# Kernel optimization log

Hardware: AMD Instinct MI355X
Metric: run time of the kernel (lower is better)

## Reference

```python
import jax, jax.numpy as jnp
import numpy as np

B, H, W, C, NC = 4, 64, 64, 64, 19


def setup_inputs() -> dict:
    key = jax.random.key(0)
    ks = jax.random.split(key, 12)
    s = 0.05  # small init so sigmoid scores are not saturated
    return {
        "feature": jax.random.normal(ks[0], (B, H, W, C), dtype=jnp.float32),
        "predict": jax.random.normal(ks[1], (B, H, W, NC), dtype=jnp.float32),
        # height attention params (dim = H); k_linear in source is unused (q reused as k)
        "hq_w": jax.random.normal(ks[2], (H, H), dtype=jnp.float32) * s,
        "hq_b": jnp.zeros((H,), dtype=jnp.float32),
        "hv_w": jax.random.normal(ks[3], (H, H), dtype=jnp.float32) * s,
        "hv_b": jnp.zeros((H,), dtype=jnp.float32),
        # width attention params (dim = W)
        "wq_w": jax.random.normal(ks[4], (W, W), dtype=jnp.float32) * s,
        "wq_b": jnp.zeros((W,), dtype=jnp.float32),
        "wv_w": jax.random.normal(ks[5], (W, W), dtype=jnp.float32) * s,
        "wv_b": jnp.zeros((W,), dtype=jnp.float32),
        # gating scalars (nn.Parameter(torch.zeros(1)) in source; random here to exercise path)
        "h_gate": jax.random.normal(ks[6], (1,), dtype=jnp.float32) * 0.5,
        "w_gate": jax.random.normal(ks[7], (1,), dtype=jnp.float32) * 0.5,
        # 1x1 conv num_classes -> 1 (stored as [NC, 1] matrix; 1x1 conv == per-pixel linear)
        "conv_w": jax.random.normal(ks[8], (NC, 1), dtype=jnp.float32) * s,
        "conv_b": jnp.zeros((1,), dtype=jnp.float32),
    }


def _self_atten(x, wq, bq, wv, bv, dim):
    # Source uses q_linear for BOTH q and k (k_linear dead), softmax replaced by sigmoid.
    q = x @ wq + bq                                   # [B, N, dim]
    v = x @ wv + bv                                   # [B, N, dim]
    scores = jax.nn.sigmoid(jnp.einsum('bnd,bmd->bnm', q, q) / jnp.sqrt(jnp.float32(dim)))
    return jnp.einsum('bnm,bmd->bnd', scores, v)      # [B, N, dim]


def _axial(x, hq_w, hq_b, hv_w, hv_b, wq_w, wq_b, wv_w, wv_b, h_gate, w_gate):
    b, h, w, c = x.shape
    # height attention: seq = W*C, feature dim = H
    xh = x.transpose(0, 2, 3, 1).reshape(b, w * c, h)
    xh = _self_atten(xh, hq_w, hq_b, hv_w, hv_b, h)
    xh = xh.reshape(b, w, c, h).transpose(0, 3, 1, 2)  # back to [B,H,W,C]
    x = xh * h_gate + x
    # width attention: seq = H*C, feature dim = W
    xw = x.transpose(0, 1, 3, 2).reshape(b, h * c, w)
    xw = _self_atten(xw, wq_w, wq_b, wv_w, wv_b, w)
    xw = xw.reshape(b, h, c, w).transpose(0, 1, 3, 2)  # back to [B,H,W,C]
    x = xw * w_gate + x
    return x


def reference(feature, predict, hq_w, hq_b, hv_w, hv_b, wq_w, wq_b, wv_w, wv_b,
              h_gate, w_gate, conv_w, conv_b):
    feat = feature + _axial(feature, hq_w, hq_b, hv_w, hv_b,
                            wq_w, wq_b, wv_w, wv_b, h_gate, w_gate)
    p = 1.0 - jax.nn.sigmoid(predict)                 # [B,H,W,NC]
    p = p @ conv_w + conv_b                           # 1x1 conv -> [B,H,W,1]
    return p * feat                                   # broadcast gate -> [B,H,W,C]
```

## Files before the change

kernel.cpp:

```cpp
#include <hip/hip_runtime.h>

typedef _Float16 f16x8 __attribute__((ext_vector_type(8)));
typedef __fp16   fp16x2 __attribute__((ext_vector_type(2)));
typedef float f32x16 __attribute__((ext_vector_type(16)));

__device__ __forceinline__ unsigned pkrtz(float a, float b) {
    fp16x2 h = __builtin_amdgcn_cvt_pkrtz(a, b);
    union { fp16x2 h; unsigned u; } c; c.h = h; return c.u;
}

__device__ __forceinline__ unsigned short f2h(float f) {
    _Float16 h = (_Float16)f;
    union { _Float16 h; unsigned short s; } c; c.h = h; return c.s;
}

__device__ __forceinline__ f16x8 pack8(const float* v) {
    union { unsigned u[4]; f16x8 h; } c;
    c.u[0] = pkrtz(v[0], v[1]);
    c.u[1] = pkrtz(v[2], v[3]);
    c.u[2] = pkrtz(v[4], v[5]);
    c.u[3] = pkrtz(v[6], v[7]);
    return c.h;
}

__global__ __launch_bounds__(256) void prep_kernel(
    const float* __restrict__ src,
    const float* __restrict__ wq, const float* __restrict__ bq,
    const float* __restrict__ wv, const float* __restrict__ bv,
    unsigned short* __restrict__ Qg, unsigned short* __restrict__ Vtg)
{
    __shared__ float slab[64][65];
    __shared__ float wqs[4160];
    __shared__ float wvs[4160];

    const int t  = threadIdx.x;
    const int bx = blockIdx.x, b = blockIdx.y;
    const int lane = t & 63, w = t >> 6;
    const int l32 = lane & 31, hi = lane >> 5;

    {
        const float4* wq4 = (const float4*)wq;
        const float4* wv4 = (const float4*)wv;
        float4* q4 = (float4*)wqs; float4* v4 = (float4*)wvs;
        #pragma unroll
        for (int i = 0; i < 4; ++i) {
            q4[i*256 + t] = wq4[i*256 + t];
            v4[i*256 + t] = wv4[i*256 + t];
        }
    }
    {
        const int k = t >> 2, c0 = (t & 3) << 4;
        const size_t sb = (size_t)b*262144 + (size_t)k*4096 + (size_t)bx*64 + c0;
        #pragma unroll
        for (int i = 0; i < 4; ++i)
            *(float4*)&slab[k][c0 + i*4] = *(const float4*)&src[sb + i*4];
    }
    __syncthreads();

    const int mt = w >> 1, nt = w & 1;
    f16x8 xa[4], wqb[4], wvb[4];
    #pragma unroll
    for (int s = 0; s < 4; ++s) {
        const int k0 = s*16 + hi*8;
        float av[8], qv[8], vv[8];
        #pragma unroll
        for (int jj = 0; jj < 8; ++jj) {
            av[jj] = slab[k0 + jj][mt*32 + l32];
            qv[jj] = wqs[(k0 + jj)*64 + nt*32 + l32];
            vv[jj] = wvs[(k0 + jj)*64 + nt*32 + l32];
        }
        xa[s]  = pack8(av);
        wqb[s] = pack8(qv);
        wvb[s] = pack8(vv);
    }

    f32x16 fz;
    #pragma unroll
    for (int i = 0; i < 16; ++i) fz[i] = 0.f;
    f32x16 accQ = __builtin_amdgcn_mfma_f32_32x32x16_f16(xa[0], wqb[0], fz, 0,0,0);
    f32x16 accV = __builtin_amdgcn_mfma_f32_32x32x16_f16(xa[0], wvb[0], fz, 0,0,0);
    #pragma unroll
    for (int s = 1; s < 4; ++s) {
        accQ = __builtin_amdgcn_mfma_f32_32x32x16_f16(xa[s], wqb[s], accQ, 0,0,0);
        accV = __builtin_amdgcn_mfma_f32_32x32x16_f16(xa[s], wvb[s], accV, 0,0,0);
    }

    __syncthreads();

    {
        #pragma unroll
        for (int r = 0; r < 16; ++r) {
            const int crow = mt*32 + (r&3) + 8*(r>>2) + 4*hi;
            wqs[crow*65 + nt*32 + l32] = accQ[r];
            wvs[crow*65 + nt*32 + l32] = accV[r];
        }
    }
    __syncthreads();

    const int c = t & 63, jg = t >> 6;
    float qa[16], va[16];
    #pragma unroll
    for (int jj = 0; jj < 16; ++jj) {
        qa[jj] = bq[jg*16+jj] + wqs[c*65 + jg*16 + jj];
        va[jj] = bv[jg*16+jj] + wvs[c*65 + jg*16 + jj];
    }
    const int token = bx*64 + c;
    union { unsigned u[8]; uint4 v[2]; } qp;
    #pragma unroll
    for (int jj = 0; jj < 8; ++jj) qp.u[jj] = pkrtz(qa[2*jj], qa[2*jj+1]);
    const size_t qoff = ((size_t)b*4096 + token)*64 + jg*16;
    *(uint4*)&Qg[qoff]     = qp.v[0];
    *(uint4*)&Qg[qoff + 8] = qp.v[1];
    #pragma unroll
    for (int jj = 0; jj < 16; ++jj)
        Vtg[((size_t)b*64 + jg*16 + jj)*4096 + token] = f2h(va[jj]);
}

__global__ __launch_bounds__(256) void prep_w_kernel(
    const float* __restrict__ feature, const float* __restrict__ Pin,
    const float* __restrict__ gate,
    const float* __restrict__ wq, const float* __restrict__ bq,
    const float* __restrict__ wv, const float* __restrict__ bv,
    unsigned short* __restrict__ Qg, unsigned short* __restrict__ Vtg,
    float* __restrict__ x1out, int nsplit)
{
    __shared__ float slab[64][65];
    __shared__ float wqs[4160];
    __shared__ float wvs[4160];

    const int t  = threadIdx.x;
    const int bx = blockIdx.x, b = blockIdx.y;
    const int lane = t & 63, w = t >> 6;
    const int l32 = lane & 31, hi = lane >> 5;

    {
        const float4* wq4 = (const float4*)wq;
        const float4* wv4 = (const float4*)wv;
        float4* q4 = (float4*)wqs; float4* v4 = (float4*)wvs;
        #pragma unroll
        for (int i = 0; i < 4; ++i) {
            q4[i*256 + t] = wq4[i*256 + t];
            v4[i*256 + t] = wv4[i*256 + t];
        }
    }
    {
        const int k = t >> 2, c0 = (t & 3) << 4;
        const size_t off = (size_t)bx*4096 + (size_t)k*64 + c0;
        const size_t fb  = (size_t)b*262144 + off;
        const float g = gate[0];
        #pragma unroll
        for (int i = 0; i < 4; ++i) {
            float4 v  = *(const float4*)&feature[fb + i*4];
            float sx = 0.f, sy = 0.f, sz = 0.f, sw = 0.f;
            for (int ks = 0; ks < nsplit; ++ks) {
                float4 pk = *(const float4*)&Pin[((size_t)(ks*4 + b) << 18) + off + i*4];
                sx += pk.x; sy += pk.y; sz += pk.z; sw += pk.w;
            }
            v.x += g * sx; v.y += g * sy; v.z += g * sz; v.w += g * sw;
            *(float4*)&slab[k][c0 + i*4] = v;
            *(float4*)&x1out[fb + i*4] = v;
        }
    }
    __syncthreads();

    const int mt = w >> 1, nt = w & 1;
    f16x8 xa[4], wqb[4], wvb[4];
    #pragma unroll
    for (int s = 0; s < 4; ++s) {
        const int k0 = s*16 + hi*8;
        float av[8], qv[8], vv[8];
        #pragma unroll
        for (int jj = 0; jj < 8; ++jj) {
            av[jj] = slab[k0 + jj][mt*32 + l32];
            qv[jj] = wqs[(k0 + jj)*64 + nt*32 + l32];
            vv[jj] = wvs[(k0 + jj)*64 + nt*32 + l32];
        }
        xa[s]  = pack8(av);
        wqb[s] = pack8(qv);
        wvb[s] = pack8(vv);
    }

    f32x16 fz;
    #pragma unroll
    for (int i = 0; i < 16; ++i) fz[i] = 0.f;
    f32x16 accQ = __builtin_amdgcn_mfma_f32_32x32x16_f16(xa[0], wqb[0], fz, 0,0,0);
    f32x16 accV = __builtin_amdgcn_mfma_f32_32x32x16_f16(xa[0], wvb[0], fz, 0,0,0);
    #pragma unroll
    for (int s = 1; s < 4; ++s) {
        accQ = __builtin_amdgcn_mfma_f32_32x32x16_f16(xa[s], wqb[s], accQ, 0,0,0);
        accV = __builtin_amdgcn_mfma_f32_32x32x16_f16(xa[s], wvb[s], accV, 0,0,0);
    }

    __syncthreads();

    {
        #pragma unroll
        for (int r = 0; r < 16; ++r) {
            const int crow = mt*32 + (r&3) + 8*(r>>2) + 4*hi;
            wqs[crow*65 + nt*32 + l32] = accQ[r];
            wvs[crow*65 + nt*32 + l32] = accV[r];
        }
    }
    __syncthreads();

    const int c = t & 63, jg = t >> 6;
    float qa[16], va[16];
    #pragma unroll
    for (int jj = 0; jj < 16; ++jj) {
        qa[jj] = bq[jg*16+jj] + wqs[c*65 + jg*16 + jj];
        va[jj] = bv[jg*16+jj] + wvs[c*65 + jg*16 + jj];
    }
    const int token = bx*64 + c;
    union { unsigned u[8]; uint4 v[2]; } qp;
    #pragma unroll
    for (int jj = 0; jj < 8; ++jj) qp.u[jj] = pkrtz(qa[2*jj], qa[2*jj+1]);
    const size_t qoff = ((size_t)b*4096 + token)*64 + jg*16;
    *(uint4*)&Qg[qoff]     = qp.v[0];
    *(uint4*)&Qg[qoff + 8] = qp.v[1];
    #pragma unroll
    for (int jj = 0; jj < 16; ++jj)
        Vtg[((size_t)b*64 + jg*16 + jj)*4096 + token] = f2h(va[jj]);
}

__global__ __launch_bounds__(256) void attn_kernel(
    const unsigned short* __restrict__ Qg,
    const unsigned short* __restrict__ Vtg,
    float* __restrict__ P)
{
    __shared__ unsigned short Ksh[2][64][72];
    __shared__ unsigned short Vts[2][64][72];

    const int t = threadIdx.x;
    const int flat = blockIdx.x + 32*(blockIdx.y + 4*blockIdx.z);
    const int xcd  = flat & 7;
    const int slot = flat >> 3;
    const int mb   = slot & 31;
    const int grp  = xcd + ((slot >> 5) << 3);
    const int b      = grp >> 2;
    const int ksplit = grp & 3;
    const int niter = 16;
    const int keybase = ksplit * 1024;
    const int lane = t & 63, w = t >> 6;
    const int l32 = lane & 31, hi = lane >> 5;

    const unsigned short* Qbase = Qg  + (size_t)b*262144;
    const unsigned short* Vbase = Vtg + (size_t)b*262144;

    f16x8 qb[4];
    {
        const unsigned short* qrow = Qbase + (size_t)(mb*128 + w*32 + l32)*64 + hi*8;
        const _Float16 sc = (_Float16)(-0.180336880f);
        #pragma unroll
        for (int s = 0; s < 4; ++s) {
            f16x8 q = *(const f16x8*)(qrow + s*16);
            qb[s] = q * sc;
        }
    }

    f32x16 fz;
    #pragma unroll
    for (int i = 0; i < 16; ++i) fz[i] = 0.f;

    f32x16 y[2];
    y[0] = fz; y[1] = fz;

    const int lrow = t >> 2;
    const int loff = (t & 3) << 4;
    {
        const uint4* gk = (const uint4*)(Qbase + (size_t)(keybase + lrow)*64 + loff);
        uint4 k0 = gk[0], k1 = gk[1];
        const uint4* gv = (const uint4*)(Vbase + (size_t)lrow*4096 + keybase + loff);
        uint4 v0 = gv[0], v1 = gv[1];
        *(uint4*)&Ksh[0][lrow][loff]     = k0;
        *(uint4*)&Ksh[0][lrow][loff + 8] = k1;
        uint4 pa = { v0.x, v0.y, v1.x, v1.y };
        uint4 pb = { v0.z, v0.w, v1.z, v1.w };
        *(uint4*)&Vts[0][lrow][loff]     = pa;
        *(uint4*)&Vts[0][lrow][loff + 8] = pb;
    }
    __syncthreads();

    for (int kb = 0; kb < niter; ++kb) {
        const int cur = kb & 1, nxt = cur ^ 1;

        uint4 nk0 = {0,0,0,0}, nk1 = {0,0,0,0}, nv0 = {0,0,0,0}, nv1 = {0,0,0,0};
        if (kb < niter - 1) {
            const int keyn = keybase + (kb + 1)*64;
            const uint4* gk = (const uint4*)(Qbase + (size_t)(keyn + lrow)*64 + loff);
            nk0 = gk[0]; nk1 = gk[1];
            const uint4* gv = (const uint4*)(Vbase + (size_t)lrow*4096 + keyn + loff);
            nv0 = gv[0]; nv1 = gv[1];
        }

        f32x16 tt[2];
        #pragma unroll
        for (int s = 0; s < 4; ++s) {
            const int co = s*16 + hi*8;
            f16x8 ka0 = *(const f16x8*)&Ksh[cur][l32][co];
            f16x8 ka1 = *(const f16x8*)&Ksh[cur][32 + l32][co];
            if (s == 0) {
                tt[0] = __builtin_amdgcn_mfma_f32_32x32x16_f16(ka0, qb[0], fz, 0,0,0);
                tt[1] = __builtin_amdgcn_mfma_f32_32x32x16_f16(ka1, qb[0], fz, 0,0,0);
            } else {
                tt[0] = __builtin_amdgcn_mfma_f32_32x32x16_f16(ka0, qb[s], tt[0], 0,0,0);
                tt[1] = __builtin_amdgcn_mfma_f32_32x32x16_f16(ka1, qb[s], tt[1], 0,0,0);
            }
        }

        #pragma unroll
        for (int u = 0; u < 2; ++u) {
            unsigned pk_[8];
            #pragma unroll
            for (int pr = 0; pr < 8; ++pr) {
                float t0 = __builtin_fminf(tt[u][2*pr+0], 60.0f);
                float t1 = __builtin_fminf(tt[u][2*pr+1], 60.0f);
                float e0 = __builtin_exp2f(t0);
                float e1 = __builtin_exp2f(t1);
                float d0 = 1.0f + e0, d1 = 1.0f + e1;
                float rr = __builtin_amdgcn_rcpf(d0 * d1);
                pk_[pr] = pkrtz(rr * d1, rr * d0);
            }
            #pragma unroll
            for (int sp = 0; sp < 2; ++sp) {
                union { unsigned u4[4]; f16x8 v; } sa;
                sa.u4[0] = pk_[sp*4 + 0];
                sa.u4[1] = pk_[sp*4 + 1];
                sa.u4[2] = pk_[sp*4 + 2];
                sa.u4[3] = pk_[sp*4 + 3];
                const int ks = u*2 + sp;
                const int co = ks*16 + hi*8;
                f16x8 vb0 = *(const f16x8*)&Vts[cur][l32][co];
                f16x8 vb1 = *(const f16x8*)&Vts[cur][32 + l32][co];
                y[0] = __builtin_amdgcn_mfma_f32_32x32x16_f16(sa.v, vb0, y[0], 0,0,0);
                y[1] = __builtin_amdgcn_mfma_f32_32x32x16_f16(sa.v, vb1, y[1], 0,0,0);
            }
        }

        if (kb < niter - 1) {
            *(uint4*)&Ksh[nxt][lrow][loff]     = nk0;
            *(uint4*)&Ksh[nxt][lrow][loff + 8] = nk1;
            uint4 pa = { nv0.x, nv0.y, nv1.x, nv1.y };
            uint4 pb = { nv0.z, nv0.w, nv1.z, nv1.w };
            *(uint4*)&Vts[nxt][lrow][loff]     = pa;
            *(uint4*)&Vts[nxt][lrow][loff + 8] = pb;
        }
        __syncthreads();
    }

    float* Pp = P + (((size_t)(ksplit*4 + b)) << 18);
    const int token0 = mb*128 + w*32 + hi*4;
    #pragma unroll
    for (int dt = 0; dt < 2; ++dt) {
        const int d = dt*32 + l32;
        #pragma unroll
        for (int g = 0; g < 4; ++g) {
            float4 v;
            v.x = y[dt][4*g+0]; v.y = y[dt][4*g+1];
            v.z = y[dt][4*g+2]; v.w = y[dt][4*g+3];
            *(float4*)&Pp[(size_t)d*4096 + token0 + 8*g] = v;
        }
    }
}

__global__ __launch_bounds__(256) void final_kernel(
    const float* __restrict__ feature, const float* __restrict__ x1,
    const float* __restrict__ Pin, const float* __restrict__ predict,
    const float* __restrict__ conv_w, const float* __restrict__ conv_b,
    const float* __restrict__ gate, float* __restrict__ out, int nsplit)
{
    const int i4 = blockIdx.x * 256 + threadIdx.x;
    const int j = i4 << 2;
    const int pix = j >> 6;
    const float* row = predict + (size_t)pix * 19;
    float pv = conv_b[0];
    #pragma unroll
    for (int i = 0; i < 19; ++i) {
        float sg = __builtin_amdgcn_rcpf(1.0f + __builtin_exp2f(-1.442695041f * row[i]));
        pv += (1.0f - sg) * conv_w[i];
    }

    const int b = j >> 18, h = (j >> 12) & 63, d = (j >> 6) & 63, c = j & 63;
    const size_t pif = ((size_t)(b*64 + d) << 12) + h*64 + c;
    float sx = 0.f, sy = 0.f, sz = 0.f, sw = 0.f;
    for (int ks = 0; ks < nsplit; ++ks) {
        float4 pk = *(const float4*)&Pin[((size_t)ks << 20) + pif];
        sx += pk.x; sy += pk.y; sz += pk.z; sw += pk.w;
    }
    const float g = gate[0];
    float4 f = ((const float4*)feature)[i4];
    float4 x = ((const float4*)x1)[i4];
    float4 o;
    o.x = pv * (f.x + x.x + g * sx);
    o.y = pv * (f.y + x.y + g * sy);
    o.z = pv * (f.z + x.z + g * sz);
    o.w = pv * (f.w + x.w + g * sw);
    ((float4*)out)[i4] = o;
}

extern "C" void kernel_launch(void* const* d_in, const int* in_sizes, int n_in,
                              void* d_out, int out_size, void* d_ws, size_t ws_size,
                              hipStream_t stream) {
    const float* feature = (const float*)d_in[0];
    const float* predict = (const float*)d_in[1];
    const float* hq_w = (const float*)d_in[2];
    const float* hq_b = (const float*)d_in[3];
    const float* hv_w = (const float*)d_in[4];
    const float* hv_b = (const float*)d_in[5];
    const float* wq_w = (const float*)d_in[6];
    const float* wq_b = (const float*)d_in[7];
    const float* wv_w = (const float*)d_in[8];
    const float* wv_b = (const float*)d_in[9];
    const float* h_gate = (const float*)d_in[10];
    const float* w_gate = (const float*)d_in[11];
    const float* conv_w = (const float*)d_in[12];
    const float* conv_b = (const float*)d_in[13];
    float* out = (float*)d_out;

    char* ws = (char*)d_ws;
    unsigned short* Qg  = (unsigned short*)(ws);
    unsigned short* Vtg = (unsigned short*)(ws + (2u << 20));
    float*          x1  = (float*)(ws + (4u << 20));
    float*          P   = (float*)(ws + (8u << 20));
    const int nsplit = 4;

    dim3 blk(256);
    prep_kernel<<<dim3(64, 4), blk, 0, stream>>>(feature, hq_w, hq_b, hv_w, hv_b,
                                                 Qg, Vtg);
    attn_kernel<<<dim3(32, 4, 4), blk, 0, stream>>>(Qg, Vtg, P);
    prep_w_kernel<<<dim3(64, 4), blk, 0, stream>>>(feature, P, h_gate,
                                                   wq_w, wq_b, wv_w, wv_b,
                                                   Qg, Vtg, x1, nsplit);
    attn_kernel<<<dim3(32, 4, 4), blk, 0, stream>>>(Qg, Vtg, P);
    final_kernel<<<dim3(1024), blk, 0, stream>>>(feature, x1, P, predict,
                                                 conv_w, conv_b, w_gate, out, nsplit);
}
```

Baseline: 191.9 us.

## Load K and V operands directly from global memory instead of LDS double-buffering

The attention kernel drops the shared-memory double buffer for K and V tiles. Each wave now loads its MFMA operands straight from global memory (through cache) every iteration, which removes the LDS stores and reads and the per-iteration __syncthreads. The cost is that each wave in a block fetches the same K/V data redundantly, with smaller 8-byte V loads, and there is no explicit prefetch to hide global latency behind compute.

Result: slower. 288.2 us (+50.2%).

```diff
diff --git a/kernel.cpp b/kernel.cpp
--- a/kernel.cpp
+++ b/kernel.cpp
@@ -227,9 +227,6 @@
     const unsigned short* __restrict__ Vtg,
     float* __restrict__ P)
 {
-    __shared__ unsigned short Ksh[2][64][72];
-    __shared__ unsigned short Vts[2][64][72];
-
     const int t = threadIdx.x;
     const int flat = blockIdx.x + 32*(blockIdx.y + 4*blockIdx.z);
     const int xcd  = flat & 7;
@@ -264,46 +261,36 @@
     f32x16 y[2];
     y[0] = fz; y[1] = fz;
 
-    const int lrow = t >> 2;
-    const int loff = (t & 3) << 4;
-    {
-        const uint4* gk = (const uint4*)(Qbase + (size_t)(keybase + lrow)*64 + loff);
-        uint4 k0 = gk[0], k1 = gk[1];
-        const uint4* gv = (const uint4*)(Vbase + (size_t)lrow*4096 + keybase + loff);
-        uint4 v0 = gv[0], v1 = gv[1];
-        *(uint4*)&Ksh[0][lrow][loff]     = k0;
-        *(uint4*)&Ksh[0][lrow][loff + 8] = k1;
-        uint4 pa = { v0.x, v0.y, v1.x, v1.y };
-        uint4 pb = { v0.z, v0.w, v1.z, v1.w };
-        *(uint4*)&Vts[0][lrow][loff]     = pa;
-        *(uint4*)&Vts[0][lrow][loff + 8] = pb;
-    }
-    __syncthreads();
+    const unsigned short* Krow0 = Qbase + (size_t)(keybase + l32)*64 + hi*8;
+    const unsigned short* Krow1 = Qbase + (size_t)(keybase + 32 + l32)*64 + hi*8;
+    const unsigned short* Vrow0 = Vbase + (size_t)l32*4096 + keybase + hi*4;
+    const unsigned short* Vrow1 = Vbase + (size_t)(32 + l32)*4096 + keybase + hi*4;
 
     for (int kb = 0; kb < niter; ++kb) {
-        const int cur = kb & 1, nxt = cur ^ 1;
-
-        uint4 nk0 = {0,0,0,0}, nk1 = {0,0,0,0}, nv0 = {0,0,0,0}, nv1 = {0,0,0,0};
-        if (kb < niter - 1) {
-            const int keyn = keybase + (kb + 1)*64;
-            const uint4* gk = (const uint4*)(Qbase + (size_t)(keyn + lrow)*64 + loff);
-            nk0 = gk[0]; nk1 = gk[1];
-            const uint4* gv = (const uint4*)(Vbase + (size_t)lrow*4096 + keyn + loff);
-            nv0 = gv[0]; nv1 = gv[1];
+        f16x8 ka0[4], ka1[4];
+        #pragma unroll
+        for (int s = 0; s < 4; ++s) {
+            ka0[s] = *(const f16x8*)(Krow0 + s*16);
+            ka1[s] = *(const f16x8*)(Krow1 + s*16);
+        }
+        union { uint2 p[2]; f16x8 v; } vb0[4], vb1[4];
+        #pragma unroll
+        for (int ks = 0; ks < 4; ++ks) {
+            vb0[ks].p[0] = *(const uint2*)(Vrow0 + ks*16);
+            vb0[ks].p[1] = *(const uint2*)(Vrow0 + ks*16 + 8);
+            vb1[ks].p[0] = *(const uint2*)(Vrow1 + ks*16);
+            vb1[ks].p[1] = *(const uint2*)(Vrow1 + ks*16 + 8);
         }
 
         f32x16 tt[2];
         #pragma unroll
         for (int s = 0; s < 4; ++s) {
-            const int co = s*16 + hi*8;
-            f16x8 ka0 = *(const f16x8*)&Ksh[cur][l32][co];
-            f16x8 ka1 = *(const f16x8*)&Ksh[cur][32 + l32][co];
             if (s == 0) {
-                tt[0] = __builtin_amdgcn_mfma_f32_32x32x16_f16(ka0, qb[0], fz, 0,0,0);
-                tt[1] = __builtin_amdgcn_mfma_f32_32x32x16_f16(ka1, qb[0], fz, 0,0,0);
+                tt[0] = __builtin_amdgcn_mfma_f32_32x32x16_f16(ka0[0], qb[0], fz, 0,0,0);
+                tt[1] = __builtin_amdgcn_mfma_f32_32x32x16_f16(ka1[0], qb[0], fz, 0,0,0);
             } else {
-                tt[0] = __builtin_amdgcn_mfma_f32_32x32x16_f16(ka0, qb[s], tt[0], 0,0,0);
-                tt[1] = __builtin_amdgcn_mfma_f32_32x32x16_f16(ka1, qb[s], tt[1], 0,0,0);
+                tt[0] = __builtin_amdgcn_mfma_f32_32x32x16_f16(ka0[s], qb[s], tt[0], 0,0,0);
+                tt[1] = __builtin_amdgcn_mfma_f32_32x32x16_f16(ka1[s], qb[s], tt[1], 0,0,0);
             }
         }
 
@@ -328,23 +315,13 @@
                 sa.u4[2] = pk_[sp*4 + 2];
                 sa.u4[3] = pk_[sp*4 + 3];
                 const int ks = u*2 + sp;
-                const int co = ks*16 + hi*8;
-                f16x8 vb0 = *(const f16x8*)&Vts[cur][l32][co];
-                f16x8 vb1 = *(const f16x8*)&Vts[cur][32 + l32][co];
-                y[0] = __builtin_amdgcn_mfma_f32_32x32x16_f16(sa.v, vb0, y[0], 0,0,0);
-                y[1] = __builtin_amdgcn_mfma_f32_32x32x16_f16(sa.v, vb1, y[1], 0,0,0);
+                y[0] = __builtin_amdgcn_mfma_f32_32x32x16_f16(sa.v, vb0[ks].v, y[0], 0,0,0);
+                y[1] = __builtin_amdgcn_mfma_f32_32x32x16_f16(sa.v, vb1[ks].v, y[1], 0,0,0);
             }
         }
 
-        if (kb < niter - 1) {
-            *(uint4*)&Ksh[nxt][lrow][loff]     = nk0;
-            *(uint4*)&Ksh[nxt][lrow][loff + 8] = nk1;
-            uint4 pa = { nv0.x, nv0.y, nv1.x, nv1.y };
-            uint4 pb = { nv0.z, nv0.w, nv1.z, nv1.w };
-            *(uint4*)&Vts[nxt][lrow][loff]     = pa;
-            *(uint4*)&Vts[nxt][lrow][loff + 8] = pb;
-        }
-        __syncthreads();
+        Krow0 += 64*64; Krow1 += 64*64;
+        Vrow0 += 64;    Vrow1 += 64;
     }
 
     float* Pp = P + (((size_t)(ksplit*4 + b)) << 18);
```
